# Kernel optimization log

Hardware: AMD Instinct MI355X
Metric: run time of the kernel (lower is better)

## Reference

```python
import jax, jax.numpy as jnp
import numpy as np

N_NODES = 20000
N_EDGES = 320000
L = 512   # input feature dim (size_dict['small'][0])
D = 256   # hidden dim (feat_channel), heads=1 so head_dim = 256
C = 2     # n_classes


def setup_inputs() -> dict:
    key = jax.random.key(0)
    ks = jax.random.split(key, 18)
    s = 0.02
    inp = {
        "x": jax.random.normal(ks[0], (N_NODES, L), jnp.float32),
        "edge_index": jax.random.randint(ks[1], (2, N_EDGES), 0, N_NODES, dtype=jnp.int32),
        "label": 1,
        # TransformerConv(L, D, heads=1): query/key/value + root skip projections
        "Wq": jax.random.normal(ks[2], (L, D), jnp.float32) * s,
        "bq": jax.random.normal(ks[3], (D,), jnp.float32) * s,
        "Wk": jax.random.normal(ks[4], (L, D), jnp.float32) * s,
        "bk": jax.random.normal(ks[5], (D,), jnp.float32) * s,
        "Wv": jax.random.normal(ks[6], (L, D), jnp.float32) * s,
        "bv": jax.random.normal(ks[7], (D,), jnp.float32) * s,
        "Ws": jax.random.normal(ks[8], (L, D), jnp.float32) * s,
        "bs": jax.random.normal(ks[9], (D,), jnp.float32) * s,
        # GlobalAdaptPooling: tanh-MLP attention (heads = n_classes) + per-class classifier
        "Wa1": jax.random.normal(ks[10], (D, D), jnp.float32) * s,
        "ba1": jax.random.normal(ks[11], (D,), jnp.float32) * s,
        "Wa2": jax.random.normal(ks[12], (D, C), jnp.float32) * s,
        "ba2": jax.random.normal(ks[13], (C,), jnp.float32) * s,
        "Wc": jax.random.normal(ks[14], (C, D), jnp.float32) * s,
        "bc": jax.random.normal(ks[15], (C,), jnp.float32) * s,
    }
    return inp


def _forward(x, edge_index, label, Wq, bq, Wk, bk, Wv, bv, Ws, bs, Wa1, ba1, Wa2, ba2, Wc, bc):
    n = x.shape[0]
    src = edge_index[0]  # message source j
    dst = edge_index[1]  # message target i
    # --- TransformerConv (heads=1, concat, root_weight=True) ---
    q = x @ Wq + bq                      # [N, D]
    k = x @ Wk + bk
    v = x @ Wv + bv
    score = jnp.sum(q[dst] * k[src], axis=-1) / jnp.sqrt(jnp.float32(D))  # [E]
    # segment softmax over incoming edges of each target node
    m = jax.ops.segment_max(score, dst, num_segments=n)
    e = jnp.exp(score - m[dst])
    den = jax.ops.segment_sum(e, dst, num_segments=n)
    alpha = e / den[dst]                 # [E]
    agg = jax.ops.segment_sum(alpha[:, None] * v[src], dst, num_segments=n)  # [N, D]
    h = agg + x @ Ws + bs
    # --- act: GELU (torch exact/erf) ---
    h = jax.nn.gelu(h, approximate=False)
    # --- GlobalAdaptPooling: node attention with n_classes heads ---
    scores = jnp.tanh(h @ Wa1 + ba1) @ Wa2 + ba2      # [N, C]
    attn = jax.nn.softmax(scores, axis=0)             # softmax over nodes
    M = attn.T @ h                                    # [C, D] per-class bag embedding
    logits = (jnp.sum(M * Wc, axis=1) + bc)[None, :]  # [1, C]
    Y_prob = jax.nn.softmax(logits, axis=1)
    A = attn[:, label]                                # [N] attention for target class
    return logits, Y_prob, A


def reference(x, edge_index, label, Wq, bq, Wk, bk, Wv, bv, Ws, bs, Wa1, ba1, Wa2, ba2, Wc, bc):
    return _forward(x, edge_index, label, Wq, bq, Wk, bk, Wv, bv, Ws, bs, Wa1, ba1, Wa2, ba2, Wc, bc)
```

## Files before the change

kernel.cpp:

```cpp
#include <hip/hip_runtime.h>
#include <hip/hip_bf16.h>
#include <math.h>

typedef float f32x4_t __attribute__((ext_vector_type(4)));
typedef float f32x2_t __attribute__((ext_vector_type(2)));
typedef __bf16 bf16x8_t __attribute__((ext_vector_type(8)));

__device__ __forceinline__ float bf2f(unsigned int u){
  union { float f; unsigned int i; } x; x.i = u << 16; return x.f;
}
__device__ __forceinline__ unsigned short f2bf(float f){
  unsigned int x = __float_as_uint(f);
  unsigned int r = (x + 0x7fffu + ((x >> 16) & 1u)) >> 16;
  return (unsigned short)r;
}
__device__ __forceinline__ unsigned int pk2bf(float a, float b){
  return (unsigned int)f2bf(a) | ((unsigned int)f2bf(b) << 16);
}
__device__ __forceinline__ void unp8s(uint4 w, float* f, float s){
  f[0] = bf2f(w.x & 0xffffu) * s; f[1] = bf2f(w.x >> 16) * s;
  f[2] = bf2f(w.y & 0xffffu) * s; f[3] = bf2f(w.y >> 16) * s;
  f[4] = bf2f(w.z & 0xffffu) * s; f[5] = bf2f(w.z >> 16) * s;
  f[6] = bf2f(w.w & 0xffffu) * s; f[7] = bf2f(w.w >> 16) * s;
}
__device__ __forceinline__ void unpf8(unsigned int w, float* f){
  f32x2_t lo = __builtin_amdgcn_cvt_pk_f32_fp8(w, false);
  f32x2_t hi = __builtin_amdgcn_cvt_pk_f32_fp8(w, true);
  f[0] = lo[0]; f[1] = lo[1]; f[2] = hi[0]; f[3] = hi[1];
}

#define GLOAD16(gsrc, ldst) \
  __builtin_amdgcn_global_load_lds((const __attribute__((address_space(1))) unsigned int*)(gsrc), \
                                   (__attribute__((address_space(3))) unsigned int*)(ldst), 16, 0, 0)

__global__ void pack_weights(const float* __restrict__ Wq, const float* __restrict__ Wk,
                             const float* __restrict__ Wv, const float* __restrict__ Ws,
                             const float* __restrict__ bq, const float* __restrict__ bk,
                             const float* __restrict__ bv, const float* __restrict__ bs,
                             unsigned short* __restrict__ wcatT, float* __restrict__ bcat){
  int idx = blockIdx.x * 256 + threadIdx.x;
  if (idx < 1024 * 512){
    int c = idx >> 9, k = idx & 511;
    int sel = c >> 8, cc = c & 255;
    const float* W = (sel == 0) ? Wq : (sel == 1) ? Wk : (sel == 2) ? Wv : Ws;
    wcatT[idx] = f2bf(W[k * 256 + cc]);
  }
  if (idx < 1024){
    int sel = idx >> 8, cc = idx & 255;
    const float* B = (sel == 0) ? bq : (sel == 1) ? bk : (sel == 2) ? bv : bs;
    bcat[idx] = B[cc];
  }
}

__global__ void pack_wa1(const float* __restrict__ Wa1, unsigned short* __restrict__ wa1T){
  int idx = blockIdx.x * 256 + threadIdx.x;
  int c = idx >> 8, k = idx & 255;
  wa1T[idx] = f2bf(Wa1[k * 256 + c]);
}

__global__ __launch_bounds__(256) void gemm_qkvs(const float* __restrict__ x,
                                                 const unsigned short* __restrict__ wcatT,
                                                 const float* __restrict__ bcat,
                                                 unsigned short* __restrict__ qbf,
                                                 unsigned short* __restrict__ sbf,
                                                 unsigned char* __restrict__ kv8,
                                                 int n_nodes, int mblocks){
  __shared__ __align__(16) unsigned char smem[128 * 272];
  unsigned short* As = (unsigned short*)smem;
  unsigned short* Bs = (unsigned short*)(smem + 8192);
  const int tid = threadIdx.x;
  const int lane = tid & 63, wave = tid >> 6;
  const int wm = wave >> 1, wn = wave & 1;
  const int g = (blockIdx.x & 7) * mblocks + (blockIdx.x >> 3);
  const int m_blk = g >> 3, n_blk = g & 7;
  const int m0 = m_blk * 128, n0 = n_blk * 128;
  const int arow = tid >> 1;
  const int acol = (tid & 1) * 16;
  const float* aptr = x + (size_t)min(m0 + arow, n_nodes - 1) * 512 + acol;
  unsigned short* adst = &As[arow * 32 + acol];
  const int brow = n0 + wave * 16 + (lane >> 2);
  const int bcol = (lane & 3) * 8;
  const int r = lane & 15, ko = (lane >> 4) * 8, ng = lane >> 4;
  f32x4_t acc[4][4] = {};
  for (int k0 = 0; k0 < 512; k0 += 32){
    GLOAD16(wcatT + (size_t)brow * 512 + k0 + bcol, &Bs[wave * 512]);
    GLOAD16(wcatT + (size_t)(brow + 64) * 512 + k0 + bcol, &Bs[(wave + 4) * 512]);
    float4 f0 = *reinterpret_cast<const float4*>(aptr + k0);
    float4 f1 = *reinterpret_cast<const float4*>(aptr + k0 + 4);
    float4 f2 = *reinterpret_cast<const float4*>(aptr + k0 + 8);
    float4 f3 = *reinterpret_cast<const float4*>(aptr + k0 + 12);
    uint4 o0, o1;
    o0.x = pk2bf(f0.x, f0.y); o0.y = pk2bf(f0.z, f0.w);
    o0.z = pk2bf(f1.x, f1.y); o0.w = pk2bf(f1.z, f1.w);
    o1.x = pk2bf(f2.x, f2.y); o1.y = pk2bf(f2.z, f2.w);
    o1.z = pk2bf(f3.x, f3.y); o1.w = pk2bf(f3.z, f3.w);
    *reinterpret_cast<uint4*>(adst) = o0;
    *reinterpret_cast<uint4*>(adst + 8) = o1;
    __syncthreads();
    bf16x8_t a[4], b[4];
    #pragma unroll
    for (int mi = 0; mi < 4; mi++)
      a[mi] = *reinterpret_cast<const bf16x8_t*>(&As[(wm * 64 + mi * 16 + r) * 32 + ko]);
    #pragma unroll
    for (int ni = 0; ni < 4; ni++)
      b[ni] = *reinterpret_cast<const bf16x8_t*>(&Bs[(wn * 64 + ni * 16 + r) * 32 + ko]);
    #pragma unroll
    for (int mi = 0; mi < 4; mi++)
      #pragma unroll
      for (int ni = 0; ni < 4; ni++)
        acc[mi][ni] = __builtin_amdgcn_mfma_f32_16x16x32_bf16(b[ni], a[mi], acc[mi][ni], 0, 0, 0);
    __syncthreads();
  }
  const bool isQ = (n_blk < 2), isS = (n_blk >= 6);
  if (isQ || isS){
    unsigned short* St = (unsigned short*)smem;
    #pragma unroll
    for (int mi = 0; mi < 4; mi++){
      #pragma unroll
      for (int ni = 0; ni < 4; ni++){
        int ml = wm * 64 + mi * 16 + r;
        int nl = wn * 64 + ni * 16 + ng * 4;
        float4 bb = *reinterpret_cast<const float4*>(&bcat[n0 + nl]);
        uint2 w;
        w.x = pk2bf(acc[mi][ni][0] + bb.x, acc[mi][ni][1] + bb.y);
        w.y = pk2bf(acc[mi][ni][2] + bb.z, acc[mi][ni][3] + bb.w);
        *reinterpret_cast<uint2*>(&St[ml * 136 + nl]) = w;
      }
    }
    __syncthreads();
    unsigned short* outp = isQ ? qbf : sbf;
    const int colhalf = isQ ? n_blk : (n_blk - 6);
    #pragma unroll
    for (int it = 0; it < 8; it++){
      int t = it * 256 + tid;
      int row = t >> 4, seg = (t & 15) * 8;
      int node = m0 + row;
      if (node < n_nodes){
        uint4 v = *reinterpret_cast<const uint4*>(&St[row * 136 + seg]);
        *reinterpret_cast<uint4*>(outp + (size_t)node * 256 + colhalf * 128 + seg) = v;
      }
    }
  } else {
    unsigned char* St = smem;
    #pragma unroll
    for (int mi = 0; mi < 4; mi++){
      #pragma unroll
      for (int ni = 0; ni < 4; ni++){
        int ml = wm * 64 + mi * 16 + r;
        int nl = wn * 64 + ni * 16 + ng * 4;
        float4 bb = *reinterpret_cast<const float4*>(&bcat[n0 + nl]);
        int u = 0;
        u = __builtin_amdgcn_cvt_pk_fp8_f32(acc[mi][ni][0] + bb.x, acc[mi][ni][1] + bb.y, u, false);
        u = __builtin_amdgcn_cvt_pk_fp8_f32(acc[mi][ni][2] + bb.z, acc[mi][ni][3] + bb.w, u, true);
        *reinterpret_cast<unsigned int*>(&St[ml * 144 + nl]) = (unsigned int)u;
      }
    }
    __syncthreads();
    #pragma unroll
    for (int it = 0; it < 4; it++){
      int t = it * 256 + tid;
      int row = t >> 3, seg = (t & 7) * 16;
      int node = m0 + row;
      if (node < n_nodes){
        uint4 v = *reinterpret_cast<const uint4*>(&St[row * 144 + seg]);
        *reinterpret_cast<uint4*>(kv8 + (size_t)node * 512 + (n_blk - 2) * 128 + seg) = v;
      }
    }
  }
}

__global__ void degree_hist(const int* __restrict__ ei, int* __restrict__ deg, int ne){
  int i = blockIdx.x * 256 + threadIdx.x;
  if (i < ne) atomicAdd(&deg[ei[ne + i]], 1);
}

__global__ void scan_deg(const int* __restrict__ deg, int* __restrict__ rowstart, int n, int ne){
  __shared__ int sm[1024];
  int tid = threadIdx.x;
  int per = (n + 1023) / 1024;
  int start = tid * per;
  int sum = 0;
  for (int i = 0; i < per; i++){
    int idx = start + i;
    sum += (idx < n) ? deg[idx] : 0;
  }
  sm[tid] = sum; __syncthreads();
  for (int off = 1; off < 1024; off <<= 1){
    int t = (tid >= off) ? sm[tid - off] : 0;
    __syncthreads();
    sm[tid] += t;
    __syncthreads();
  }
  int run = sm[tid] - sum;
  for (int i = 0; i < per; i++){
    int idx = start + i;
    if (idx < n){
      rowstart[idx] = run;
      run += deg[idx];
    }
  }
  if (tid == 0) rowstart[n] = ne;
}

__global__ void scatter_edges(const int* __restrict__ ei, const int* __restrict__ rowstart,
                              int* __restrict__ cursor, int* __restrict__ csrsrc, int ne){
  int i = blockIdx.x * 256 + threadIdx.x;
  if (i < ne){
    int d = ei[ne + i];
    int pos = atomicAdd(&cursor[d], 1);
    csrsrc[rowstart[d] + pos] = ei[i] << 9;
  }
}

__global__ __launch_bounds__(256) void edge_attn(const unsigned short* __restrict__ qbf,
                                                 const unsigned short* __restrict__ sbf,
                                                 const unsigned char* __restrict__ kv8,
                                                 const int* __restrict__ rowstart,
                                                 const int* __restrict__ csrsrc,
                                                 unsigned short* __restrict__ hbf, int n_nodes){
  const int tid = threadIdx.x;
  const int lane = tid & 63, wave = tid >> 6;
  const int g = lane >> 4, t = lane & 15;
  const int node = blockIdx.x * 16 + wave * 4 + g;
  const bool active = node < n_nodes;
  const int nd = active ? node : 0;
  const float qs = 0.0625f * 1.44269504088896340736f;
  float q[16];
  {
    const unsigned short* qp = qbf + (size_t)nd * 256 + t * 16;
    uint4 w0 = *reinterpret_cast<const uint4*>(qp);
    uint4 w1 = *reinterpret_cast<const uint4*>(qp + 8);
    unp8s(w0, q, qs); unp8s(w1, q + 8, qs);
  }
  int rs = rowstart[nd];
  int re = active ? rowstart[nd + 1] : rs;
  float m = -1e30f, den = 0.f;
  float acc[16];
  #pragma unroll
  for (int j = 0; j < 16; j++) acc[j] = 0.f;
  for (int i = rs; i < re; i++){
    int soff = csrsrc[i];
    const unsigned char* kb = kv8 + (size_t)soff + t * 16;
    uint4 kw = *reinterpret_cast<const uint4*>(kb);
    float kf[16];
    unpf8(kw.x, kf); unpf8(kw.y, kf + 4); unpf8(kw.z, kf + 8); unpf8(kw.w, kf + 12);
    float s = 0.f;
    #pragma unroll
    for (int j = 0; j < 16; j++) s = fmaf(q[j], kf[j], s);
    s += __shfl_xor(s, 1); s += __shfl_xor(s, 2);
    s += __shfl_xor(s, 4); s += __shfl_xor(s, 8);
    uint4 vw = *reinterpret_cast<const uint4*>(kb + 256);
    float vf[16];
    unpf8(vw.x, vf); unpf8(vw.y, vf + 4); unpf8(vw.z, vf + 8); unpf8(vw.w, vf + 12);
    if (s > m){
      float sc = exp2f(m - s);
      den = den * sc + 1.0f;
      #pragma unroll
      for (int j = 0; j < 16; j++) acc[j] = fmaf(acc[j], sc, vf[j]);
      m = s;
    } else {
      float e = exp2f(s - m);
      den += e;
      #pragma unroll
      for (int j = 0; j < 16; j++) acc[j] = fmaf(e, vf[j], acc[j]);
    }
  }
  float inv = (den > 0.f) ? 1.f / den : 0.f;
  const unsigned short* sp = sbf + (size_t)nd * 256 + t * 16;
  uint4 s0 = *reinterpret_cast<const uint4*>(sp);
  uint4 s1 = *reinterpret_cast<const uint4*>(sp + 8);
  float sf[16]; unp8s(s0, sf, 1.0f); unp8s(s1, sf + 8, 1.0f);
  const float inv_sqrt2 = 0.70710678118654752f;
  unsigned int o[8];
  #pragma unroll
  for (int j = 0; j < 8; j++){
    float h0 = acc[2 * j] * inv + sf[2 * j];
    float h1 = acc[2 * j + 1] * inv + sf[2 * j + 1];
    h0 = 0.5f * h0 * (1.f + erff(h0 * inv_sqrt2));
    h1 = 0.5f * h1 * (1.f + erff(h1 * inv_sqrt2));
    o[j] = (unsigned int)f2bf(h0) | ((unsigned int)f2bf(h1) << 16);
  }
  if (active){
    uint4* dst = reinterpret_cast<uint4*>(hbf + (size_t)node * 256 + t * 16);
    dst[0] = make_uint4(o[0], o[1], o[2], o[3]);
    dst[1] = make_uint4(o[4], o[5], o[6], o[7]);
  }
}

__global__ __launch_bounds__(256) void mlp_mfma(const unsigned short* __restrict__ hbf,
                                                const unsigned short* __restrict__ wa1T,
                                                const float* __restrict__ ba1,
                                                const float* __restrict__ Wa2,
                                                const float* __restrict__ ba2,
                                                float* __restrict__ s2, int n_nodes){
  __shared__ __align__(16) unsigned short As[64 * 72];
  __shared__ float s2s[64][2];
  const int tid = threadIdx.x;
  const int lane = tid & 63, wave = tid >> 6;
  const int m0 = blockIdx.x * 64;
  const int c0 = wave * 64;
  const int r = lane & 15, rg = (lane >> 4) * 4;
  if (tid < 128) s2s[tid >> 1][tid & 1] = 0.f;
  f32x4_t acc[4][4] = {};
  for (int k0 = 0; k0 < 256; k0 += 64){
    int arow = tid >> 2, akc = (tid & 3) * 16;
    uint4 a0v = make_uint4(0,0,0,0), a1v = make_uint4(0,0,0,0);
    if (m0 + arow < n_nodes){
      const unsigned short* src = hbf + (size_t)(m0 + arow) * 256 + k0 + akc;
      a0v = *reinterpret_cast<const uint4*>(src);
      a1v = *reinterpret_cast<const uint4*>(src + 8);
    }
    *reinterpret_cast<uint4*>(&As[arow * 72 + akc]) = a0v;
    *reinterpret_cast<uint4*>(&As[arow * 72 + akc + 8]) = a1v;
    __syncthreads();
    #pragma unroll
    for (int kk = 0; kk < 2; kk++){
      int kg = kk * 32 + (lane >> 4) * 8;
      bf16x8_t a[4], b[4];
      #pragma unroll
      for (int mi = 0; mi < 4; mi++)
        a[mi] = *reinterpret_cast<const bf16x8_t*>(&As[(mi * 16 + r) * 72 + kg]);
      #pragma unroll
      for (int ni = 0; ni < 4; ni++)
        b[ni] = *reinterpret_cast<const bf16x8_t*>(wa1T + (size_t)(c0 + ni * 16 + r) * 256 + k0 + kg);
      #pragma unroll
      for (int mi = 0; mi < 4; mi++)
        #pragma unroll
        for (int ni = 0; ni < 4; ni++)
          acc[mi][ni] = __builtin_amdgcn_mfma_f32_16x16x32_bf16(a[mi], b[ni], acc[mi][ni], 0, 0, 0);
    }
    __syncthreads();
  }
  float w20[4], w21[4], b1c[4];
  #pragma unroll
  for (int ni = 0; ni < 4; ni++){
    int col = c0 + ni * 16 + r;
    w20[ni] = Wa2[col * 2]; w21[ni] = Wa2[col * 2 + 1]; b1c[ni] = ba1[col];
  }
  #pragma unroll
  for (int mi = 0; mi < 4; mi++){
    #pragma unroll
    for (int j = 0; j < 4; j++){
      float t0 = 0.f, t1 = 0.f;
      #pragma unroll
      for (int ni = 0; ni < 4; ni++){
        float t = tanhf(acc[mi][ni][j] + b1c[ni]);
        t0 += t * w20[ni]; t1 += t * w21[ni];
      }
      t0 += __shfl_xor(t0, 1); t0 += __shfl_xor(t0, 2);
      t0 += __shfl_xor(t0, 4); t0 += __shfl_xor(t0, 8);
      t1 += __shfl_xor(t1, 1); t1 += __shfl_xor(t1, 2);
      t1 += __shfl_xor(t1, 4); t1 += __shfl_xor(t1, 8);
      if (r == 0){
        int row = mi * 16 + rg + j;
        atomicAdd(&s2s[row][0], t0);
        atomicAdd(&s2s[row][1], t1);
      }
    }
  }
  __syncthreads();
  if (tid < 128){
    int row = tid >> 1, c = tid & 1;
    int node = m0 + row;
    if (node < n_nodes) s2[node * 2 + c] = s2s[row][c] + ba2[c];
  }
}

__global__ void col_reduce(const float* __restrict__ s2, float* __restrict__ red, int n){
  __shared__ float sm[1024];
  __shared__ float mshare[2];
  int tid = threadIdx.x;
  float mx0 = -INFINITY, mx1 = -INFINITY;
  for (int i = tid; i < n; i += 1024){
    mx0 = fmaxf(mx0, s2[2 * i]);
    mx1 = fmaxf(mx1, s2[2 * i + 1]);
  }
  sm[tid] = mx0; __syncthreads();
  for (int off = 512; off > 0; off >>= 1){
    if (tid < off) sm[tid] = fmaxf(sm[tid], sm[tid + off]);
    __syncthreads();
  }
  if (tid == 0) mshare[0] = sm[0];
  __syncthreads();
  sm[tid] = mx1; __syncthreads();
  for (int off = 512; off > 0; off >>= 1){
    if (tid < off) sm[tid] = fmaxf(sm[tid], sm[tid + off]);
    __syncthreads();
  }
  if (tid == 0) mshare[1] = sm[0];
  __syncthreads();
  float m0 = mshare[0], m1 = mshare[1];
  float s0 = 0.f, s1 = 0.f;
  for (int i = tid; i < n; i += 1024){
    s0 += expf(s2[2 * i] - m0);
    s1 += expf(s2[2 * i + 1] - m1);
  }
  sm[tid] = s0; __syncthreads();
  for (int off = 512; off > 0; off >>= 1){
    if (tid < off) sm[tid] += sm[tid + off];
    __syncthreads();
  }
  float den0 = sm[0];
  __syncthreads();
  sm[tid] = s1; __syncthreads();
  for (int off = 512; off > 0; off >>= 1){
    if (tid < off) sm[tid] += sm[tid + off];
    __syncthreads();
  }
  if (tid == 0){
    red[0] = m0; red[1] = m1; red[2] = den0; red[3] = sm[0];
  }
}

__global__ __launch_bounds__(256) void attn_M(const float* __restrict__ s2, const float* __restrict__ red,
                                              const unsigned short* __restrict__ hbf, const int* __restrict__ label,
                                              float* __restrict__ Mbuf, float* __restrict__ outA, int n){
  __shared__ float a0s[256], a1s[256];
  int tid = threadIdx.x;
  int n0 = blockIdx.x * 256;
  int node = n0 + tid;
  float m0 = red[0], m1 = red[1];
  float i0 = 1.f / red[2], i1 = 1.f / red[3];
  float a0 = 0.f, a1 = 0.f;
  if (node < n){
    a0 = expf(s2[2 * node] - m0) * i0;
    a1 = expf(s2[2 * node + 1] - m1) * i1;
    outA[node] = (label[0] == 0) ? a0 : a1;
  }
  a0s[tid] = a0; a1s[tid] = a1;
  __syncthreads();
  int d = tid;
  float M0 = 0.f, M1 = 0.f;
  int cnt = min(256, n - n0);
  for (int i = 0; i < cnt; i++){
    float hv = bf2f((unsigned int)hbf[(size_t)(n0 + i) * 256 + d]);
    M0 += a0s[i] * hv;
    M1 += a1s[i] * hv;
  }
  atomicAdd(&Mbuf[d], M0);
  atomicAdd(&Mbuf[256 + d], M1);
}

__global__ void final_k(const float* __restrict__ Mbuf, const float* __restrict__ Wc,
                        const float* __restrict__ bc, float* __restrict__ out){
  __shared__ float sm[256];
  __shared__ float l0s;
  int tid = threadIdx.x;
  float p0 = Mbuf[tid] * Wc[tid];
  float p1 = Mbuf[256 + tid] * Wc[256 + tid];
  sm[tid] = p0; __syncthreads();
  for (int off = 128; off > 0; off >>= 1){
    if (tid < off) sm[tid] += sm[tid + off];
    __syncthreads();
  }
  if (tid == 0) l0s = sm[0];
  __syncthreads();
  sm[tid] = p1; __syncthreads();
  for (int off = 128; off > 0; off >>= 1){
    if (tid < off) sm[tid] += sm[tid + off];
    __syncthreads();
  }
  if (tid == 0){
    float l0 = l0s + bc[0];
    float l1 = sm[0] + bc[1];
    out[0] = l0; out[1] = l1;
    float mx = fmaxf(l0, l1);
    float e0 = expf(l0 - mx), e1 = expf(l1 - mx);
    float inv = 1.f / (e0 + e1);
    out[2] = e0 * inv; out[3] = e1 * inv;
  }
}

extern "C" void kernel_launch(void* const* d_in, const int* in_sizes, int n_in,
                              void* d_out, int out_size, void* d_ws, size_t ws_size,
                              hipStream_t stream) {
  const float* x   = (const float*)d_in[0];
  const int*   ei  = (const int*)d_in[1];
  const int*   lab = (const int*)d_in[2];
  const float* Wq  = (const float*)d_in[3];
  const float* bq  = (const float*)d_in[4];
  const float* Wk  = (const float*)d_in[5];
  const float* bk  = (const float*)d_in[6];
  const float* Wv  = (const float*)d_in[7];
  const float* bv  = (const float*)d_in[8];
  const float* Ws  = (const float*)d_in[9];
  const float* bs  = (const float*)d_in[10];
  const float* Wa1 = (const float*)d_in[11];
  const float* ba1 = (const float*)d_in[12];
  const float* Wa2 = (const float*)d_in[13];
  const float* ba2 = (const float*)d_in[14];
  const float* Wc  = (const float*)d_in[15];
  const float* bc  = (const float*)d_in[16];
  float* out = (float*)d_out;

  const int n  = in_sizes[0] / 512;
  const int ne = in_sizes[1] / 2;

  char* ws = (char*)d_ws;
  size_t off = 0;
  auto take = [&](size_t bytes){ size_t r = off; off += (bytes + 255) & ~(size_t)255; return r; };
  unsigned short* wcatT  = (unsigned short*)(ws + take((size_t)1024 * 512 * 2));
  float*          bcat   = (float*)(ws + take(1024 * 4));
  unsigned short* qbf    = (unsigned short*)(ws + take((size_t)n * 256 * 2));
  unsigned short* sbf    = (unsigned short*)(ws + take((size_t)n * 256 * 2));
  unsigned char*  kv8    = (unsigned char*)(ws + take((size_t)n * 512));
  unsigned short* hbf    = (unsigned short*)(ws + take((size_t)n * 256 * 2));
  unsigned short* wa1T   = (unsigned short*)(ws + take((size_t)256 * 256 * 2));
  float*          s2     = (float*)(ws + take((size_t)n * 2 * 4));
  size_t zoff = off;
  int*            deg    = (int*)(ws + take((size_t)n * 4));
  int*            cursor = (int*)(ws + take((size_t)n * 4));
  float*          Mbuf   = (float*)(ws + take(512 * 4));
  size_t zlen = off - zoff;
  int*            rowst  = (int*)(ws + take((size_t)(n + 1) * 4));
  int*            csrsrc = (int*)(ws + take((size_t)ne * 4));
  float*          red    = (float*)(ws + take(4 * 4));

  hipMemsetAsync(ws + zoff, 0, zlen, stream);

  pack_weights<<<(1024 * 512 + 255) / 256, 256, 0, stream>>>(Wq, Wk, Wv, Ws, bq, bk, bv, bs, wcatT, bcat);
  pack_wa1<<<256, 256, 0, stream>>>(Wa1, wa1T);
  const int mblocks = (n + 127) / 128;
  gemm_qkvs<<<8 * mblocks, 256, 0, stream>>>(x, wcatT, bcat, qbf, sbf, kv8, n, mblocks);
  degree_hist<<<(ne + 255) / 256, 256, 0, stream>>>(ei, deg, ne);
  scan_deg<<<1, 1024, 0, stream>>>(deg, rowst, n, ne);
  scatter_edges<<<(ne + 255) / 256, 256, 0, stream>>>(ei, rowst, cursor, csrsrc, ne);
  edge_attn<<<(n + 15) / 16, 256, 0, stream>>>(qbf, sbf, kv8, rowst, csrsrc, hbf, n);
  mlp_mfma<<<(n + 63) / 64, 256, 0, stream>>>(hbf, wa1T, ba1, Wa2, ba2, s2, n);
  col_reduce<<<1, 1024, 0, stream>>>(s2, red, n);
  attn_M<<<(n + 255) / 256, 256, 0, stream>>>(s2, red, hbf, lab, Mbuf, out + 4, n);
  final_k<<<1, 256, 0, stream>>>(Mbuf, Wc, bc, out);
  (void)ws_size; (void)out_size; (void)n_in;
}
```

Before: 218.9 us.

## Swizzle GEMM LDS layout, prefetch A tile, and shrink epilogue staging buffer

The QKVS projection GEMM now stores its A and B tiles in LDS with an XOR swizzle to avoid bank conflicts when the MFMA operands are read. The packed weight matrix is pre-swizzled in global memory so the direct global-to-LDS loads land in the swizzled layout. The fp32 x loads for the next k-step are issued after the barrier, so they are in flight during the MFMAs. The epilogue stages output in two 64-row halves, which shrinks shared memory to raise occupancy, at the cost of extra barriers.

```diff
diff --git a/kernel.cpp b/kernel.cpp
--- a/kernel.cpp
+++ b/kernel.cpp
@@ -17,6 +17,8 @@
 __device__ __forceinline__ unsigned int pk2bf(float a, float b){
   return (unsigned int)f2bf(a) | ((unsigned int)f2bf(b) << 16);
 }
+__device__ __forceinline__ int swz4(int r){ return (r ^ (r >> 2) ^ (r >> 4)) & 3; }
+
 __device__ __forceinline__ void unp8s(uint4 w, float* f, float s){
   f[0] = bf2f(w.x & 0xffffu) * s; f[1] = bf2f(w.x >> 16) * s;
   f[2] = bf2f(w.y & 0xffffu) * s; f[3] = bf2f(w.y >> 16) * s;
@@ -43,7 +45,9 @@
     int c = idx >> 9, k = idx & 511;
     int sel = c >> 8, cc = c & 255;
     const float* W = (sel == 0) ? Wq : (sel == 1) ? Wk : (sel == 2) ? Wv : Ws;
-    wcatT[idx] = f2bf(W[k * 256 + cc]);
+    int p = ((k >> 3) & 3) ^ swz4(c & 127);
+    int dst = c * 512 + (k & ~31) + p * 8 + (k & 7);
+    wcatT[dst] = f2bf(W[k * 256 + cc]);
   }
   if (idx < 1024){
     int sel = idx >> 8, cc = idx & 255;
@@ -65,7 +69,7 @@
                                                  unsigned short* __restrict__ sbf,
                                                  unsigned char* __restrict__ kv8,
                                                  int n_nodes, int mblocks){
-  __shared__ __align__(16) unsigned char smem[128 * 272];
+  __shared__ __align__(16) unsigned char smem[17408];
   unsigned short* As = (unsigned short*)smem;
   unsigned short* Bs = (unsigned short*)(smem + 8192);
   const int tid = threadIdx.x;
@@ -75,35 +79,45 @@
   const int m_blk = g >> 3, n_blk = g & 7;
   const int m0 = m_blk * 128, n0 = n_blk * 128;
   const int arow = tid >> 1;
-  const int acol = (tid & 1) * 16;
-  const float* aptr = x + (size_t)min(m0 + arow, n_nodes - 1) * 512 + acol;
-  unsigned short* adst = &As[arow * 32 + acol];
+  const int au0 = (tid & 1) * 2;
+  const int ap0 = (au0 ^ swz4(arow)) * 8;
+  const int ap1 = ((au0 + 1) ^ swz4(arow)) * 8;
+  const float* aptr = x + (size_t)min(m0 + arow, n_nodes - 1) * 512 + au0 * 8;
   const int brow = n0 + wave * 16 + (lane >> 2);
   const int bcol = (lane & 3) * 8;
-  const int r = lane & 15, ko = (lane >> 4) * 8, ng = lane >> 4;
+  const int r = lane & 15, q4 = lane >> 4;
+  int aoff[4], boff[4];
+  #pragma unroll
+  for (int mi = 0; mi < 4; mi++){ int rr = wm * 64 + mi * 16 + r; aoff[mi] = rr * 32 + ((q4 ^ swz4(rr)) * 8); }
+  #pragma unroll
+  for (int ni = 0; ni < 4; ni++){ int rb = wn * 64 + ni * 16 + r; boff[ni] = rb * 32 + ((q4 ^ swz4(rb)) * 8); }
   f32x4_t acc[4][4] = {};
+  float4 af0 = *reinterpret_cast<const float4*>(aptr);
+  float4 af1 = *reinterpret_cast<const float4*>(aptr + 4);
+  float4 af2 = *reinterpret_cast<const float4*>(aptr + 8);
+  float4 af3 = *reinterpret_cast<const float4*>(aptr + 12);
   for (int k0 = 0; k0 < 512; k0 += 32){
     GLOAD16(wcatT + (size_t)brow * 512 + k0 + bcol, &Bs[wave * 512]);
     GLOAD16(wcatT + (size_t)(brow + 64) * 512 + k0 + bcol, &Bs[(wave + 4) * 512]);
-    float4 f0 = *reinterpret_cast<const float4*>(aptr + k0);
-    float4 f1 = *reinterpret_cast<const float4*>(aptr + k0 + 4);
-    float4 f2 = *reinterpret_cast<const float4*>(aptr + k0 + 8);
-    float4 f3 = *reinterpret_cast<const float4*>(aptr + k0 + 12);
     uint4 o0, o1;
-    o0.x = pk2bf(f0.x, f0.y); o0.y = pk2bf(f0.z, f0.w);
-    o0.z = pk2bf(f1.x, f1.y); o0.w = pk2bf(f1.z, f1.w);
-    o1.x = pk2bf(f2.x, f2.y); o1.y = pk2bf(f2.z, f2.w);
-    o1.z = pk2bf(f3.x, f3.y); o1.w = pk2bf(f3.z, f3.w);
-    *reinterpret_cast<uint4*>(adst) = o0;
-    *reinterpret_cast<uint4*>(adst + 8) = o1;
-    __syncthreads();
+    o0.x = pk2bf(af0.x, af0.y); o0.y = pk2bf(af0.z, af0.w);
+    o0.z = pk2bf(af1.x, af1.y); o0.w = pk2bf(af1.z, af1.w);
+    o1.x = pk2bf(af2.x, af2.y); o1.y = pk2bf(af2.z, af2.w);
+    o1.z = pk2bf(af3.x, af3.y); o1.w = pk2bf(af3.z, af3.w);
+    *reinterpret_cast<uint4*>(&As[arow * 32 + ap0]) = o0;
+    *reinterpret_cast<uint4*>(&As[arow * 32 + ap1]) = o1;
+    __syncthreads();
+    if (k0 + 32 < 512){
+      af0 = *reinterpret_cast<const float4*>(aptr + k0 + 32);
+      af1 = *reinterpret_cast<const float4*>(aptr + k0 + 36);
+      af2 = *reinterpret_cast<const float4*>(aptr + k0 + 40);
+      af3 = *reinterpret_cast<const float4*>(aptr + k0 + 44);
+    }
     bf16x8_t a[4], b[4];
     #pragma unroll
-    for (int mi = 0; mi < 4; mi++)
-      a[mi] = *reinterpret_cast<const bf16x8_t*>(&As[(wm * 64 + mi * 16 + r) * 32 + ko]);
-    #pragma unroll
-    for (int ni = 0; ni < 4; ni++)
-      b[ni] = *reinterpret_cast<const bf16x8_t*>(&Bs[(wn * 64 + ni * 16 + r) * 32 + ko]);
+    for (int mi = 0; mi < 4; mi++) a[mi] = *reinterpret_cast<const bf16x8_t*>(&As[aoff[mi]]);
+    #pragma unroll
+    for (int ni = 0; ni < 4; ni++) b[ni] = *reinterpret_cast<const bf16x8_t*>(&Bs[boff[ni]]);
     #pragma unroll
     for (int mi = 0; mi < 4; mi++)
       #pragma unroll
@@ -114,57 +128,69 @@
   const bool isQ = (n_blk < 2), isS = (n_blk >= 6);
   if (isQ || isS){
     unsigned short* St = (unsigned short*)smem;
-    #pragma unroll
-    for (int mi = 0; mi < 4; mi++){
-      #pragma unroll
-      for (int ni = 0; ni < 4; ni++){
-        int ml = wm * 64 + mi * 16 + r;
-        int nl = wn * 64 + ni * 16 + ng * 4;
-        float4 bb = *reinterpret_cast<const float4*>(&bcat[n0 + nl]);
-        uint2 w;
-        w.x = pk2bf(acc[mi][ni][0] + bb.x, acc[mi][ni][1] + bb.y);
-        w.y = pk2bf(acc[mi][ni][2] + bb.z, acc[mi][ni][3] + bb.w);
-        *reinterpret_cast<uint2*>(&St[ml * 136 + nl]) = w;
-      }
-    }
-    __syncthreads();
     unsigned short* outp = isQ ? qbf : sbf;
     const int colhalf = isQ ? n_blk : (n_blk - 6);
     #pragma unroll
-    for (int it = 0; it < 8; it++){
-      int t = it * 256 + tid;
-      int row = t >> 4, seg = (t & 15) * 8;
-      int node = m0 + row;
-      if (node < n_nodes){
-        uint4 v = *reinterpret_cast<const uint4*>(&St[row * 136 + seg]);
-        *reinterpret_cast<uint4*>(outp + (size_t)node * 256 + colhalf * 128 + seg) = v;
+    for (int ch = 0; ch < 2; ch++){
+      if (wm == ch){
+        #pragma unroll
+        for (int mi = 0; mi < 4; mi++){
+          #pragma unroll
+          for (int ni = 0; ni < 4; ni++){
+            int mloc = mi * 16 + r;
+            int nl = wn * 64 + ni * 16 + q4 * 4;
+            float4 bb = *reinterpret_cast<const float4*>(&bcat[n0 + nl]);
+            uint2 w;
+            w.x = pk2bf(acc[mi][ni][0] + bb.x, acc[mi][ni][1] + bb.y);
+            w.y = pk2bf(acc[mi][ni][2] + bb.z, acc[mi][ni][3] + bb.w);
+            *reinterpret_cast<uint2*>(&St[mloc * 136 + nl]) = w;
+          }
+        }
       }
+      __syncthreads();
+      #pragma unroll
+      for (int it = 0; it < 4; it++){
+        int u = it * 256 + tid;
+        int row = u >> 4, seg = (u & 15) * 8;
+        int node = m0 + ch * 64 + row;
+        if (node < n_nodes){
+          uint4 v = *reinterpret_cast<const uint4*>(&St[row * 136 + seg]);
+          *reinterpret_cast<uint4*>(outp + (size_t)node * 256 + colhalf * 128 + seg) = v;
+        }
+      }
+      __syncthreads();
     }
   } else {
-    unsigned char* St = smem;
-    #pragma unroll
-    for (int mi = 0; mi < 4; mi++){
-      #pragma unroll
-      for (int ni = 0; ni < 4; ni++){
-        int ml = wm * 64 + mi * 16 + r;
-        int nl = wn * 64 + ni * 16 + ng * 4;
-        float4 bb = *reinterpret_cast<const float4*>(&bcat[n0 + nl]);
-        int u = 0;
-        u = __builtin_amdgcn_cvt_pk_fp8_f32(acc[mi][ni][0] + bb.x, acc[mi][ni][1] + bb.y, u, false);
-        u = __builtin_amdgcn_cvt_pk_fp8_f32(acc[mi][ni][2] + bb.z, acc[mi][ni][3] + bb.w, u, true);
-        *reinterpret_cast<unsigned int*>(&St[ml * 144 + nl]) = (unsigned int)u;
+    unsigned char* St8 = smem;
+    #pragma unroll
+    for (int ch = 0; ch < 2; ch++){
+      if (wm == ch){
+        #pragma unroll
+        for (int mi = 0; mi < 4; mi++){
+          #pragma unroll
+          for (int ni = 0; ni < 4; ni++){
+            int mloc = mi * 16 + r;
+            int nl = wn * 64 + ni * 16 + q4 * 4;
+            float4 bb = *reinterpret_cast<const float4*>(&bcat[n0 + nl]);
+            int u = 0;
+            u = __builtin_amdgcn_cvt_pk_fp8_f32(acc[mi][ni][0] + bb.x, acc[mi][ni][1] + bb.y, u, false);
+            u = __builtin_amdgcn_cvt_pk_fp8_f32(acc[mi][ni][2] + bb.z, acc[mi][ni][3] + bb.w, u, true);
+            *reinterpret_cast<unsigned int*>(&St8[mloc * 144 + nl]) = (unsigned int)u;
+          }
+        }
       }
-    }
-    __syncthreads();
-    #pragma unroll
-    for (int it = 0; it < 4; it++){
-      int t = it * 256 + tid;
-      int row = t >> 3, seg = (t & 7) * 16;
-      int node = m0 + row;
-      if (node < n_nodes){
-        uint4 v = *reinterpret_cast<const uint4*>(&St[row * 144 + seg]);
-        *reinterpret_cast<uint4*>(kv8 + (size_t)node * 512 + (n_blk - 2) * 128 + seg) = v;
+      __syncthreads();
+      #pragma unroll
+      for (int it = 0; it < 2; it++){
+        int u = it * 256 + tid;
+        int row = u >> 3, seg = (u & 7) * 16;
+        int node = m0 + ch * 64 + row;
+        if (node < n_nodes){
+          uint4 v = *reinterpret_cast<const uint4*>(&St8[row * 144 + seg]);
+          *reinterpret_cast<uint4*>(kv8 + (size_t)node * 512 + (n_blk - 2) * 128 + seg) = v;
+        }
       }
+      __syncthreads();
     }
   }
 }
```

After: 233.9 us. 1.07x slower.
